# Optimization experiments

Hardware: AMD Instinct MI355X
Metric: run time of the kernel (lower is better)

## Reference

```python
import jax, jax.numpy as jnp
import numpy as np

B = 4096        # graphs
N0 = 32         # nodes per graph
N = B * N0      # 131072 nodes
EP = 128        # edges per graph
E = B * EP      # 524288 edges
H, C = 2, 64    # heads, per-head channels
D = H * C       # 128
K1, K2, K3 = 29, 27, 25  # ceil(0.9*32), ceil(0.9*29), ceil(0.9*27)


def setup_inputs() -> dict:
    key = jax.random.key(0)
    ks = jax.random.split(key, 8)
    x = jax.random.normal(ks[0], (N, 41), jnp.float32)
    g = jnp.repeat(jnp.arange(B, dtype=jnp.int32), EP)
    src = g * N0 + jax.random.randint(ks[1], (E,), 0, N0, jnp.int32)
    dst = g * N0 + jax.random.randint(ks[2], (E,), 0, N0, jnp.int32)
    edge_index = jnp.stack([src, dst])
    edge_attr = jax.random.normal(ks[3], (E, 10), jnp.float32)
    batch = jnp.repeat(jnp.arange(B, dtype=jnp.int32), N0)

    def lin(k, i, o):
        return jax.random.normal(k, (i, o), jnp.float32) / np.float32(np.sqrt(i))

    p = {"x": x, "edge_index": edge_index, "edge_attr": edge_attr, "batch": batch}
    fins = {1: 41, 2: D, 3: D}
    for li in (1, 2, 3):
        sub = jax.random.split(ks[3 + li], 6)
        p[f"W{li}"] = lin(sub[0], fins[li], D)
        p[f"We{li}"] = lin(sub[1], 10, D)
        p[f"as{li}"] = jax.random.normal(sub[2], (H, C), jnp.float32) * 0.1
        p[f"ad{li}"] = jax.random.normal(sub[3], (H, C), jnp.float32) * 0.1
        p[f"ae{li}"] = jax.random.normal(sub[4], (H, C), jnp.float32) * 0.1
        p[f"b{li}"] = jnp.zeros((D,), jnp.float32)
        p[f"g{li}"] = jnp.ones((D,), jnp.float32)
        p[f"be{li}"] = jnp.zeros((D,), jnp.float32)
        p[f"pw{li}"] = jax.random.normal(sub[5], (D,), jnp.float32)
    sub = jax.random.split(ks[7], 2)
    p["fw1"] = lin(sub[0], D, 64)
    p["fb1"] = jnp.zeros((64,), jnp.float32)
    p["fw2"] = lin(sub[1], 64, 1)
    p["fb2"] = jnp.zeros((1,), jnp.float32)
    return p


def gat_conv(x, src, dst, edge_attr, node_mask, edge_mask, W, We, a_s, a_d, a_e, b):
    # PyG GATConv w/ edge_dim, add_self_loops=True, fill_value='mean'
    emf = edge_mask.astype(x.dtype)
    loop_attr = jax.ops.segment_sum(edge_attr * emf[:, None], dst, num_segments=N)
    loop_attr = loop_attr / jnp.maximum(jax.ops.segment_sum(emf, dst, num_segments=N), 1.0)[:, None]
    idx = jnp.arange(N, dtype=src.dtype)
    s = jnp.concatenate([src, idx])
    d = jnp.concatenate([dst, idx])
    ea = jnp.concatenate([edge_attr, loop_attr], axis=0)
    msk = jnp.concatenate([edge_mask, node_mask])
    h = (x @ W).reshape(N, H, C)                       # [N,H,C]
    eh = (ea @ We).reshape(-1, H, C)                   # [E+N,H,C]
    alpha = (h * a_s).sum(-1)[s] + (h * a_d).sum(-1)[d] + (eh * a_e).sum(-1)
    alpha = jax.nn.leaky_relu(alpha, 0.2)              # [E+N,H]
    alpha = jnp.where(msk[:, None], alpha, -1e9)
    mx = jax.ops.segment_max(alpha, d, num_segments=N)  # segment softmax over dst
    p = jnp.where(msk[:, None], jnp.exp(alpha - mx[d]), 0.0)
    den = jax.ops.segment_sum(p, d, num_segments=N)
    w = p / jnp.maximum(den[d], 1e-16)
    out = jax.ops.segment_sum(w[:, :, None] * h[s], d, num_segments=N)
    return out.reshape(N, D) + b


def masked_bn(x, nm, gamma, beta, eps=1e-5):
    m = nm.astype(x.dtype)[:, None]
    n = jnp.maximum(m.sum(), 1.0)
    mu = (x * m).sum(0) / n
    var = (jnp.square(x - mu) * m).sum(0) / n
    return gamma * (x - mu) * jax.lax.rsqrt(var + eps) + beta


def topk_pool(x, w, nm, k):
    sc = (x @ w) / jnp.linalg.norm(w)                  # [N]
    sg = jnp.where(nm, sc, -1e9).reshape(B, N0)
    _, idx = jax.lax.top_k(sg, k)                      # per-graph top-k
    nm2 = jnp.zeros((B, N0), bool).at[jnp.arange(B)[:, None], idx].set(True).reshape(-1)
    xn = jnp.where(nm2[:, None], x * jnp.tanh(sc)[:, None], 0.0)
    return xn, nm2


def graph_mean(x, nm, batch):
    m = nm.astype(x.dtype)
    s = jax.ops.segment_sum(x * m[:, None], batch, num_segments=B)
    c = jax.ops.segment_sum(m, batch, num_segments=B)
    return s / jnp.maximum(c, 1.0)[:, None]


def _forward(x, edge_index, edge_attr, batch,
             W1, We1, as1, ad1, ae1, b1, g1, be1, pw1,
             W2, We2, as2, ad2, ae2, b2, g2, be2, pw2,
             W3, We3, as3, ad3, ae3, b3, g3, be3, pw3,
             fw1, fb1, fw2, fb2):
    src, dst = edge_index[0], edge_index[1]
    nm = jnp.ones((N,), bool)
    em = jnp.ones((E,), bool)
    layers = [(W1, We1, as1, ad1, ae1, b1, g1, be1, pw1, K1),
              (W2, We2, as2, ad2, ae2, b2, g2, be2, pw2, K2),
              (W3, We3, as3, ad3, ae3, b3, g3, be3, pw3, K3)]
    reads = []
    for (W, We, a_s, a_d, a_e, b, g, be, pw, k) in layers:
        x = gat_conv(x, src, dst, edge_attr, nm, em, W, We, a_s, a_d, a_e, b)
        x = jax.nn.relu(masked_bn(x, nm, g, be))
        x, nm = topk_pool(x, pw, nm, k)
        em = em & nm[src] & nm[dst]
        reads.append(graph_mean(x, nm, batch))
    z = reads[0] + reads[1] + reads[2]
    z = jax.nn.relu(z @ fw1 + fb1)
    return z @ fw2 + fb2


def reference(x, edge_index, edge_attr, batch,
              W1, We1, as1, ad1, ae1, b1, g1, be1, pw1,
              W2, We2, as2, ad2, ae2, b2, g2, be2, pw2,
              W3, We3, as3, ad3, ae3, b3, g3, be3, pw3,
              fw1, fb1, fw2, fb2):
    return _forward(x, edge_index, edge_attr, batch,
                    W1, We1, as1, ad1, ae1, b1, g1, be1, pw1,
                    W2, We2, as2, ad2, ae2, b2, g2, be2, pw2,
                    W3, We3, as3, ad3, ae3, b3, g3, be3, pw3,
                    fw1, fb1, fw2, fb2)
```

## Files before the change

### kernel.cpp

```cpp
#include <hip/hip_runtime.h>

#define NN 131072
#define NG 4096
#define NE 524288

__device__ __forceinline__ float lrelu(float a){ return a>=0.f ? a : 0.2f*a; }

template<int K, int PMODE, int KSEL>
__global__ __launch_bounds__(256) void pool_gemm_kernel(
    const float* __restrict__ Xin, float* bufA, unsigned char* nmg,
    const float* __restrict__ stat,
    const float* __restrict__ gamma, const float* __restrict__ beta,
    const float* __restrict__ Wg,
    float* zacc)
{
    constexpr int XP = (K == 41) ? 44 : 132;
    __shared__ float xs[64 * XP];
    __shared__ float scS[64], tsS[64];
    __shared__ int   nmlS[64];

    int tid = threadIdx.x;
    long row0 = (long)blockIdx.x * 64;
    int g0 = blockIdx.x * 2;

    if (PMODE == 0) {
        for (int i = tid; i < 64 * 41; i += 256) {
            int r = i / 41, c = i - r * 41;
            xs[r * 44 + c] = Xin[row0 * 41 + i];
        }
    } else {
        for (int i = tid; i < 2048; i += 256) {
            int r = i >> 5, dc = (i & 31) * 4;
            float4 v = *(const float4*)&bufA[(row0 + r) * 128 + dc];
            v.x = fmaxf(gamma[dc    ] * (v.x - stat[dc    ]) * stat[128 + dc    ] + beta[dc    ], 0.f);
            v.y = fmaxf(gamma[dc + 1] * (v.y - stat[dc + 1]) * stat[128 + dc + 1] + beta[dc + 1], 0.f);
            v.z = fmaxf(gamma[dc + 2] * (v.z - stat[dc + 2]) * stat[128 + dc + 2] + beta[dc + 2], 0.f);
            v.w = fmaxf(gamma[dc + 3] * (v.w - stat[dc + 3]) * stat[128 + dc + 3] + beta[dc + 3], 0.f);
            *(float4*)&xs[r * XP + dc] = v;
        }
        if (tid < 64) nmlS[tid] = (PMODE == 1) ? 1 : (int)nmg[g0 * 32 + tid];
    }
    __syncthreads();

    if (PMODE > 0) {
        {
            int node = tid >> 2, l4 = tid & 3;
            float s = 0.f;
            for (int m = 0; m < 32; m++) { int c = l4 + 4 * m; s += xs[node * XP + c] * stat[256 + c]; }
            s += __shfl_xor(s, 2); s += __shfl_xor(s, 1);
            if (l4 == 0) scS[node] = s;
        }
        __syncthreads();
        if (tid < 64) {
            int gp = tid >> 5, n = tid & 31;
            float sn = nmlS[tid] ? scS[tid] : -1e9f;
            int cnt = 0;
            for (int j = 0; j < 32; j++) {
                float sj = nmlS[gp * 32 + j] ? scS[gp * 32 + j] : -1e9f;
                cnt += (sj > sn || (sj == sn && j < n)) ? 1 : 0;
            }
            int sl = (cnt < KSEL) ? 1 : 0;
            nmg[g0 * 32 + tid] = (unsigned char)sl;
            tsS[tid] = sl ? tanhf(scS[tid]) : 0.f;
        }
        __syncthreads();
        {
            int gp = tid >> 7, d = tid & 127;
            float s = 0.f;
            for (int n = 0; n < 32; n++) s += tsS[gp * 32 + n] * xs[(gp * 32 + n) * XP + d];
            zacc[(long)(g0 + gp) * 128 + d] += s * (1.0f / (float)KSEL);
        }
    }

    int r0 = (tid >> 5) * 8, c4 = (tid & 31) * 4;
    float acc[8][4];
#pragma unroll
    for (int i = 0; i < 8; i++)
#pragma unroll
        for (int j = 0; j < 4; j++) acc[i][j] = 0.f;

    constexpr int KM4 = (K / 4) * 4;
#pragma unroll 4
    for (int k0 = 0; k0 < KM4; k0 += 4) {
        float4 wv0 = *(const float4*)&Wg[(k0 + 0) * 128 + c4];
        float4 wv1 = *(const float4*)&Wg[(k0 + 1) * 128 + c4];
        float4 wv2 = *(const float4*)&Wg[(k0 + 2) * 128 + c4];
        float4 wv3 = *(const float4*)&Wg[(k0 + 3) * 128 + c4];
#pragma unroll
        for (int i = 0; i < 8; i++) {
            float4 xv = *(const float4*)&xs[(r0 + i) * XP + k0];
            acc[i][0] += xv.x * wv0.x + xv.y * wv1.x + xv.z * wv2.x + xv.w * wv3.x;
            acc[i][1] += xv.x * wv0.y + xv.y * wv1.y + xv.z * wv2.y + xv.w * wv3.y;
            acc[i][2] += xv.x * wv0.z + xv.y * wv1.z + xv.z * wv2.z + xv.w * wv3.z;
            acc[i][3] += xv.x * wv0.w + xv.y * wv1.w + xv.z * wv2.w + xv.w * wv3.w;
        }
    }
    for (int k = KM4; k < K; k++) {
        float4 wv = *(const float4*)&Wg[k * 128 + c4];
#pragma unroll
        for (int i = 0; i < 8; i++) {
            float xv = xs[(r0 + i) * XP + k];
            acc[i][0] += xv * wv.x; acc[i][1] += xv * wv.y;
            acc[i][2] += xv * wv.z; acc[i][3] += xv * wv.w;
        }
    }
#pragma unroll
    for (int i = 0; i < 8; i++) {
        float t = 1.f;
        if (PMODE > 0) t = tsS[r0 + i];
        *(float4*)&bufA[(row0 + r0 + i) * 128 + c4] =
            make_float4(acc[i][0] * t, acc[i][1] * t, acc[i][2] * t, acc[i][3] * t);
    }
}

__global__ __launch_bounds__(256) void attn_kernel(
    float* bufA,
    const int* __restrict__ srcp, const int* __restrict__ dstp,
    const float* __restrict__ EA,
    const unsigned char* __restrict__ nmg,
    const float* __restrict__ stat,
    const float* __restrict__ as_, const float* __restrict__ ad_,
    const float* __restrict__ bb,
    float* sums)
{
    __shared__ float hs[32 * 128];
    __shared__ float Wm[2 * 32 * 36];
    __shared__ float scr[320];
    __shared__ unsigned char nmlS[32];

    int g = blockIdx.x, tid = threadIdx.x;
    long gb = (long)g * 4096;

    float ea0 = 0.f, ea1 = 0.f;
    int myls = 0, myld = 0;
    if (tid < 128) {
        myls = srcp[g * 128 + tid] & 31;
        myld = dstp[g * 128 + tid] & 31;
        const float* ep = EA + (long)(g * 128 + tid) * 10;
#pragma unroll
        for (int j = 0; j < 10; j++) { float v = ep[j]; ea0 += v * stat[384 + j]; ea1 += v * stat[394 + j]; }
    }
    for (int i = tid; i < 2304; i += 256) Wm[i] = 0.f;
    if (tid < 96) scr[128 + tid] = 0.f;
    if (tid < 32) nmlS[tid] = nmg[g * 32 + tid];
#pragma unroll
    for (int k = 0; k < 4; k++) {
        int i = tid + 256 * k, r = i >> 5, c4 = i & 31;
        *(float4*)&hs[r * 128 + ((c4 ^ (r & 7)) << 2)] =
            *(const float4*)&bufA[gb + (long)i * 4];
    }
    __syncthreads();

    {
        int node = tid >> 3, l8 = tid & 7, rb = node * 128, k = node & 7;
        float s0 = 0, s1 = 0, d0 = 0, d1 = 0;
#pragma unroll
        for (int m = 0; m < 8; m++) {
            int c = l8 + 8 * m, c4 = c >> 2, j = c & 3;
            int o0 = rb + ((c4 ^ k) << 2) + j;
            float h0 = hs[o0], h1 = hs[o0 + 64];
            s0 += h0 * as_[c];      s1 += h1 * as_[64 + c];
            d0 += h0 * ad_[c];      d1 += h1 * ad_[64 + c];
        }
        s0 += __shfl_xor(s0, 4); s0 += __shfl_xor(s0, 2); s0 += __shfl_xor(s0, 1);
        s1 += __shfl_xor(s1, 4); s1 += __shfl_xor(s1, 2); s1 += __shfl_xor(s1, 1);
        d0 += __shfl_xor(d0, 4); d0 += __shfl_xor(d0, 2); d0 += __shfl_xor(d0, 1);
        d1 += __shfl_xor(d1, 4); d1 += __shfl_xor(d1, 2); d1 += __shfl_xor(d1, 1);
        if (l8 == 0) {
            scr[node * 2] = s0;      scr[node * 2 + 1] = s1;
            scr[64 + node * 2] = d0; scr[64 + node * 2 + 1] = d1;
        }
    }
    int mymk = 0;
    if (tid < 128) {
        mymk = (int)nmlS[myls] & (int)nmlS[myld];
        if (mymk) {
            atomicAdd(&scr[128 + myld * 2], ea0);
            atomicAdd(&scr[128 + myld * 2 + 1], ea1);
            atomicAdd(&scr[192 + myld], 1.f);
        }
    }
    __syncthreads();

    if (tid < 128) {
        if (mymk) {
            float p0 = __expf(lrelu(scr[myls * 2]     + scr[64 + myld * 2]     + ea0));
            float p1 = __expf(lrelu(scr[myls * 2 + 1] + scr[64 + myld * 2 + 1] + ea1));
            atomicAdd(&Wm[myls * 36 + myld], p0);
            atomicAdd(&Wm[1152 + myls * 36 + myld], p1);
        }
    } else if (tid < 192) {
        int t2 = tid - 128, n = t2 >> 1, h = t2 & 1;
        if (nmlS[n]) {
            float c = scr[192 + n]; c = (c > 0.f) ? c : 1.f;
            float ps = __expf(lrelu(scr[n * 2 + h] + scr[64 + n * 2 + h] + scr[128 + n * 2 + h] / c));
            atomicAdd(&Wm[h * 1152 + n * 36 + n], ps);
        }
    }
    __syncthreads();

    if (tid < 64) {
        int n = tid & 31, h = tid >> 5;
        const float* Wh = &Wm[h * 1152 + n];
        float den = 0.f;
#pragma unroll 8
        for (int s = 0; s < 32; s++) den += Wh[s * 36];
        scr[256 + h * 32 + n] = 1.f / fmaxf(den, 1e-16f);
    } else if (tid < 128) {
        *(float4*)&scr[(tid - 64) * 4] = make_float4(0.f, 0.f, 0.f, 0.f);
    }
    __syncthreads();

    {
        int d = tid & 127, h = d >> 6, nb = tid >> 7;
        int c4 = d >> 2, j = d & 3;
        const float* Wh = &Wm[h * 1152 + nb * 16];
        float acc[16];
#pragma unroll
        for (int i = 0; i < 16; i++) acc[i] = 0.f;
        for (int s = 0; s < 32; s++) {
            float hv = hs[s * 128 + ((c4 ^ (s & 7)) << 2) + j];
            float4 w0 = *(const float4*)&Wh[s * 36];
            float4 w1 = *(const float4*)&Wh[s * 36 + 4];
            float4 w2 = *(const float4*)&Wh[s * 36 + 8];
            float4 w3 = *(const float4*)&Wh[s * 36 + 12];
            acc[0]  += w0.x * hv; acc[1]  += w0.y * hv; acc[2]  += w0.z * hv; acc[3]  += w0.w * hv;
            acc[4]  += w1.x * hv; acc[5]  += w1.y * hv; acc[6]  += w1.z * hv; acc[7]  += w1.w * hv;
            acc[8]  += w2.x * hv; acc[9]  += w2.y * hv; acc[10] += w2.z * hv; acc[11] += w2.w * hv;
            acc[12] += w3.x * hv; acc[13] += w3.y * hv; acc[14] += w3.z * hv; acc[15] += w3.w * hv;
        }
        float bv = bb[d];
        float sp = 0.f, sq = 0.f;
#pragma unroll
        for (int i = 0; i < 16; i++) {
            int n = nb * 16 + i;
            float v = acc[i] * scr[256 + h * 32 + n] + bv;
            bufA[gb + n * 128 + d] = v;
            if (nmlS[n]) { sp += v; sq += v * v; }
        }
        atomicAdd(&scr[d], sp);
        atomicAdd(&scr[128 + d], sq);
    }
    __syncthreads();

    if (tid < 128) {
        int rep = (g & 31) * 256;
        atomicAdd(&sums[rep + tid], scr[tid]);
        atomicAdd(&sums[rep + 128 + tid], scr[128 + tid]);
    }
}

__global__ __launch_bounds__(128) void setup_kernel(
    float* sums, float* stat, const float* __restrict__ We, const float* __restrict__ ae)
{
    int t = threadIdx.x;
    for (int i = t; i < 32 * 256; i += 128) sums[i] = 0.f;
    if (t < 20) {
        int h = t / 10, j = t - 10 * h;
        float s = 0.f;
        for (int c = 0; c < 64; c++) s += We[j * 128 + h * 64 + c] * ae[h * 64 + c];
        stat[384 + t] = s;
    }
}

__global__ __launch_bounds__(128) void finalize_kernel(
    float* sums, float n, const float* __restrict__ pw, float* stat,
    const float* __restrict__ Wen, const float* __restrict__ aen)
{
    int d = threadIdx.x;
    float s1 = 0.f, s2 = 0.f;
#pragma unroll
    for (int r = 0; r < 32; r++) { s1 += sums[r * 256 + d]; s2 += sums[r * 256 + 128 + d]; }
    float mean = s1 / n;
    float var = s2 / n - mean * mean;
    if (var < 0.f) var = 0.f;
    float rstd = rsqrtf(var + 1e-5f);
    float p = pw[d];
    float q = p * p;
#pragma unroll
    for (int o = 32; o >= 1; o >>= 1) q += __shfl_xor(q, o);
    __shared__ float w2[2];
    if ((d & 63) == 0) w2[d >> 6] = q;
    __syncthreads();
    float nrm = sqrtf(w2[0] + w2[1]);
    stat[d] = mean; stat[128 + d] = rstd; stat[256 + d] = p / nrm;
    if (d < 20) {
        int h = d / 10, j = d - 10 * h;
        float s = 0.f;
        for (int c = 0; c < 64; c++) s += Wen[j * 128 + h * 64 + c] * aen[h * 64 + c];
        stat[384 + d] = s;
    }
    for (int i = d; i < 32 * 256; i += 128) sums[i] = 0.f;
}

__global__ __launch_bounds__(256) void final_kernel(
    const float* __restrict__ bufA, const unsigned char* __restrict__ nmg,
    const float* __restrict__ stat,
    const float* __restrict__ gamma, const float* __restrict__ beta,
    const float* __restrict__ zacc,
    const float* __restrict__ fw1, const float* __restrict__ fb1,
    const float* __restrict__ fw2, const float* __restrict__ fb2,
    float* __restrict__ out)
{
    __shared__ float xs[32 * 132], zt[128], hred[64], scS[32], tsS[32];
    __shared__ int nmlS[32];
    int g = blockIdx.x, tid = threadIdx.x;
    long gb = (long)g * 4096;

    if (tid < 32) nmlS[tid] = (int)nmg[g * 32 + tid];
    for (int i = tid; i < 1024; i += 256) {
        int r = i >> 5, dc = (i & 31) * 4;
        float4 v = *(const float4*)&bufA[gb + i * 4];
        v.x = fmaxf(gamma[dc    ] * (v.x - stat[dc    ]) * stat[128 + dc    ] + beta[dc    ], 0.f);
        v.y = fmaxf(gamma[dc + 1] * (v.y - stat[dc + 1]) * stat[128 + dc + 1] + beta[dc + 1], 0.f);
        v.z = fmaxf(gamma[dc + 2] * (v.z - stat[dc + 2]) * stat[128 + dc + 2] + beta[dc + 2], 0.f);
        v.w = fmaxf(gamma[dc + 3] * (v.w - stat[dc + 3]) * stat[128 + dc + 3] + beta[dc + 3], 0.f);
        *(float4*)&xs[r * 132 + dc] = v;
    }
    __syncthreads();

    {
        int node = tid >> 3, l8 = tid & 7;
        float s = 0.f;
        for (int m = 0; m < 16; m++) { int c = l8 + 8 * m; s += xs[node * 132 + c] * stat[256 + c]; }
        s += __shfl_xor(s, 4); s += __shfl_xor(s, 2); s += __shfl_xor(s, 1);
        if (l8 == 0) scS[node] = s;
    }
    __syncthreads();

    if (tid < 32) {
        float sn = nmlS[tid] ? scS[tid] : -1e9f;
        int cnt = 0;
        for (int j = 0; j < 32; j++) {
            float sj = nmlS[j] ? scS[j] : -1e9f;
            cnt += (sj > sn || (sj == sn && j < tid)) ? 1 : 0;
        }
        tsS[tid] = (cnt < 25) ? tanhf(scS[tid]) : 0.f;
    }
    __syncthreads();

    if (tid < 128) {
        float s = 0.f;
        for (int n = 0; n < 32; n++) s += xs[n * 132 + tid] * tsS[n];
        zt[tid] = zacc[(long)g * 128 + tid] + s * (1.0f / 25.0f);
    }
    __syncthreads();

    {
        int j = tid >> 2, p = tid & 3;
        float s = 0.f;
        for (int d = p * 32; d < p * 32 + 32; d++) s += zt[d] * fw1[d * 64 + j];
        s += __shfl_xor(s, 1); s += __shfl_xor(s, 2);
        if (p == 0) hred[j] = fmaxf(s + fb1[j], 0.f) * fw2[j];
    }
    __syncthreads();
    if (tid < 64) {
        float v = hred[tid];
#pragma unroll
        for (int o = 32; o >= 1; o >>= 1) v += __shfl_xor(v, o);
        if (tid == 0) out[g] = v + fb2[0];
    }
}

extern "C" void kernel_launch(void* const* d_in, const int* in_sizes, int n_in,
                              void* d_out, int out_size, void* d_ws, size_t ws_size,
                              hipStream_t stream)
{
    const float* X0 = (const float*)d_in[0];
    const int*   EI = (const int*)d_in[1];
    const float* EA = (const float*)d_in[2];
    const int* srcp = EI;
    const int* dstp = EI + NE;

    const float* W1  = (const float*)d_in[4];  const float* We1 = (const float*)d_in[5];
    const float* as1 = (const float*)d_in[6];  const float* ad1 = (const float*)d_in[7];
    const float* ae1 = (const float*)d_in[8];  const float* b1  = (const float*)d_in[9];
    const float* g1  = (const float*)d_in[10]; const float* be1 = (const float*)d_in[11];
    const float* pw1 = (const float*)d_in[12];
    const float* W2  = (const float*)d_in[13]; const float* We2 = (const float*)d_in[14];
    const float* as2 = (const float*)d_in[15]; const float* ad2 = (const float*)d_in[16];
    const float* ae2 = (const float*)d_in[17]; const float* b2  = (const float*)d_in[18];
    const float* g2  = (const float*)d_in[19]; const float* be2 = (const float*)d_in[20];
    const float* pw2 = (const float*)d_in[21];
    const float* W3  = (const float*)d_in[22]; const float* We3 = (const float*)d_in[23];
    const float* as3 = (const float*)d_in[24]; const float* ad3 = (const float*)d_in[25];
    const float* ae3 = (const float*)d_in[26]; const float* b3  = (const float*)d_in[27];
    const float* g3  = (const float*)d_in[28]; const float* be3 = (const float*)d_in[29];
    const float* pw3 = (const float*)d_in[30];
    const float* fw1 = (const float*)d_in[31]; const float* fb1 = (const float*)d_in[32];
    const float* fw2 = (const float*)d_in[33]; const float* fb2 = (const float*)d_in[34];

    float* bufA = (float*)d_ws;
    float* z    = bufA + (size_t)NN * 128;
    float* sums = z + (size_t)NG * 128;
    float* stat = sums + 32 * 256;
    unsigned char* nmg = (unsigned char*)(stat + 512);

    hipMemsetAsync(nmg, 1, NN, stream);
    hipMemsetAsync(z, 0, (size_t)NG * 128 * sizeof(float), stream);
    setup_kernel<<<1, 128, 0, stream>>>(sums, stat, We1, ae1);

    pool_gemm_kernel<41, 0, 1><<<NN / 64, 256, 0, stream>>>(
        X0, bufA, nmg, stat, g1, be1, W1, z);
    attn_kernel<<<NG, 256, 0, stream>>>(bufA, srcp, dstp, EA, nmg, stat, as1, ad1, b1, sums);
    finalize_kernel<<<1, 128, 0, stream>>>(sums, 131072.f, pw1, stat, We2, ae2);

    pool_gemm_kernel<128, 1, 29><<<NN / 64, 256, 0, stream>>>(
        X0, bufA, nmg, stat, g1, be1, W2, z);
    attn_kernel<<<NG, 256, 0, stream>>>(bufA, srcp, dstp, EA, nmg, stat, as2, ad2, b2, sums);
    finalize_kernel<<<1, 128, 0, stream>>>(sums, 4096.f * 29.f, pw2, stat, We3, ae3);

    pool_gemm_kernel<128, 2, 27><<<NN / 64, 256, 0, stream>>>(
        X0, bufA, nmg, stat, g2, be2, W3, z);
    attn_kernel<<<NG, 256, 0, stream>>>(bufA, srcp, dstp, EA, nmg, stat, as3, ad3, b3, sums);
    finalize_kernel<<<1, 128, 0, stream>>>(sums, 4096.f * 27.f, pw3, stat, We3, ae3);

    final_kernel<<<NG, 256, 0, stream>>>(
        bufA, nmg, stat, g3, be3, z, fw1, fb1, fw2, fb2, (float*)d_out);
}
```

Before: 545.1 us.

## Restructure pool GEMM to per-lane rows with wave-uniform scalar weight loads and swizzled LDS

The small GEMM in pool_gemm_kernel now has each lane own one row and each wave own 32 output columns. Because the wave index goes through readfirstlane, the weight reads are wave-uniform and can become scalar loads instead of per-thread float4 global loads. The shared tile drops its padding and uses an XOR swizzle on float4 columns to avoid LDS bank conflicts, and the scoring and readout loops are updated to match. The cost is 32 accumulators per thread, which raises register pressure, and row-per-lane stores of 32 contiguous floats that coalesce less well.

```diff
diff --git a/kernel.cpp b/kernel.cpp
--- a/kernel.cpp
+++ b/kernel.cpp
@@ -14,8 +14,8 @@
     const float* __restrict__ Wg,
     float* zacc)
 {
-    constexpr int XP = (K == 41) ? 44 : 132;
-    __shared__ float xs[64 * XP];
+    constexpr int XSZ = (K == 41) ? 64 * 44 : 64 * 128;
+    __shared__ float xs[XSZ];
     __shared__ float scS[64], tsS[64];
     __shared__ int   nmlS[64];
 
@@ -30,13 +30,13 @@
         }
     } else {
         for (int i = tid; i < 2048; i += 256) {
-            int r = i >> 5, dc = (i & 31) * 4;
+            int r = i >> 5, c4 = i & 31, dc = c4 * 4;
             float4 v = *(const float4*)&bufA[(row0 + r) * 128 + dc];
             v.x = fmaxf(gamma[dc    ] * (v.x - stat[dc    ]) * stat[128 + dc    ] + beta[dc    ], 0.f);
             v.y = fmaxf(gamma[dc + 1] * (v.y - stat[dc + 1]) * stat[128 + dc + 1] + beta[dc + 1], 0.f);
             v.z = fmaxf(gamma[dc + 2] * (v.z - stat[dc + 2]) * stat[128 + dc + 2] + beta[dc + 2], 0.f);
             v.w = fmaxf(gamma[dc + 3] * (v.w - stat[dc + 3]) * stat[128 + dc + 3] + beta[dc + 3], 0.f);
-            *(float4*)&xs[r * XP + dc] = v;
+            *(float4*)&xs[r * 128 + ((c4 ^ (r & 7)) << 2)] = v;
         }
         if (tid < 64) nmlS[tid] = (PMODE == 1) ? 1 : (int)nmg[g0 * 32 + tid];
     }
@@ -44,9 +44,10 @@
 
     if (PMODE > 0) {
         {
-            int node = tid >> 2, l4 = tid & 3;
+            int node = tid >> 2, l4 = tid & 3, kk = node & 7;
             float s = 0.f;
-            for (int m = 0; m < 32; m++) { int c = l4 + 4 * m; s += xs[node * XP + c] * stat[256 + c]; }
+            for (int m = 0; m < 32; m++)
+                s += xs[node * 128 + ((m ^ kk) << 2) + l4] * stat[256 + 4 * m + l4];
             s += __shfl_xor(s, 2); s += __shfl_xor(s, 1);
             if (l4 == 0) scS[node] = s;
         }
@@ -65,51 +66,72 @@
         }
         __syncthreads();
         {
-            int gp = tid >> 7, d = tid & 127;
+            int gp = tid >> 7, d = tid & 127, c4 = d >> 2, j = d & 3;
             float s = 0.f;
-            for (int n = 0; n < 32; n++) s += tsS[gp * 32 + n] * xs[(gp * 32 + n) * XP + d];
+            for (int n = 0; n < 32; n++) {
+                int r = gp * 32 + n;
+                s += tsS[r] * xs[r * 128 + ((c4 ^ (r & 7)) << 2) + j];
+            }
             zacc[(long)(g0 + gp) * 128 + d] += s * (1.0f / (float)KSEL);
         }
     }
 
-    int r0 = (tid >> 5) * 8, c4 = (tid & 31) * 4;
-    float acc[8][4];
-#pragma unroll
-    for (int i = 0; i < 8; i++)
-#pragma unroll
-        for (int j = 0; j < 4; j++) acc[i][j] = 0.f;
+    int lane = tid & 63;
+    int wv = __builtin_amdgcn_readfirstlane(tid >> 6);
+    const float* __restrict__ Wb = Wg + wv * 32;
+
+    float accv[32];
+#pragma unroll
+    for (int c = 0; c < 32; c++) accv[c] = 0.f;
 
     constexpr int KM4 = (K / 4) * 4;
-#pragma unroll 4
+#pragma unroll 2
     for (int k0 = 0; k0 < KM4; k0 += 4) {
-        float4 wv0 = *(const float4*)&Wg[(k0 + 0) * 128 + c4];
-        float4 wv1 = *(const float4*)&Wg[(k0 + 1) * 128 + c4];
-        float4 wv2 = *(const float4*)&Wg[(k0 + 2) * 128 + c4];
-        float4 wv3 = *(const float4*)&Wg[(k0 + 3) * 128 + c4];
-#pragma unroll
-        for (int i = 0; i < 8; i++) {
-            float4 xv = *(const float4*)&xs[(r0 + i) * XP + k0];
-            acc[i][0] += xv.x * wv0.x + xv.y * wv1.x + xv.z * wv2.x + xv.w * wv3.x;
-            acc[i][1] += xv.x * wv0.y + xv.y * wv1.y + xv.z * wv2.y + xv.w * wv3.y;
-            acc[i][2] += xv.x * wv0.z + xv.y * wv1.z + xv.z * wv2.z + xv.w * wv3.z;
-            acc[i][3] += xv.x * wv0.w + xv.y * wv1.w + xv.z * wv2.w + xv.w * wv3.w;
+        float4 xv;
+        if (PMODE == 0) {
+            xv = *(const float4*)&xs[lane * 44 + k0];
+        } else {
+            xv = *(const float4*)&xs[lane * 128 + ((((k0 >> 2) ^ (lane & 7))) << 2)];
+        }
+        {
+            const float* Wr = Wb + (k0 + 0) * 128;
+#pragma unroll
+            for (int c = 0; c < 32; c++) accv[c] += xv.x * Wr[c];
+        }
+        {
+            const float* Wr = Wb + (k0 + 1) * 128;
+#pragma unroll
+            for (int c = 0; c < 32; c++) accv[c] += xv.y * Wr[c];
+        }
+        {
+            const float* Wr = Wb + (k0 + 2) * 128;
+#pragma unroll
+            for (int c = 0; c < 32; c++) accv[c] += xv.z * Wr[c];
+        }
+        {
+            const float* Wr = Wb + (k0 + 3) * 128;
+#pragma unroll
+            for (int c = 0; c < 32; c++) accv[c] += xv.w * Wr[c];
         }
     }
     for (int k = KM4; k < K; k++) {
-        float4 wv = *(const float4*)&Wg[k * 128 + c4];
-#pragma unroll
-        for (int i = 0; i < 8; i++) {
-            float xv = xs[(r0 + i) * XP + k];
-            acc[i][0] += xv * wv.x; acc[i][1] += xv * wv.y;
-            acc[i][2] += xv * wv.z; acc[i][3] += xv * wv.w;
-        }
-    }
-#pragma unroll
-    for (int i = 0; i < 8; i++) {
+        float xk = (PMODE == 0)
+            ? xs[lane * 44 + k]
+            : xs[lane * 128 + (((k >> 2) ^ (lane & 7)) << 2) + (k & 3)];
+        const float* Wr = Wb + k * 128;
+#pragma unroll
+        for (int c = 0; c < 32; c++) accv[c] += xk * Wr[c];
+    }
+
+    {
         float t = 1.f;
-        if (PMODE > 0) t = tsS[r0 + i];
-        *(float4*)&bufA[(row0 + r0 + i) * 128 + c4] =
-            make_float4(acc[i][0] * t, acc[i][1] * t, acc[i][2] * t, acc[i][3] * t);
+        if (PMODE > 0) t = tsS[lane];
+        float* orow = &bufA[(row0 + lane) * 128 + wv * 32];
+#pragma unroll
+        for (int cc = 0; cc < 8; cc++)
+            *(float4*)&orow[cc * 4] = make_float4(
+                accv[cc * 4 + 0] * t, accv[cc * 4 + 1] * t,
+                accv[cc * 4 + 2] * t, accv[cc * 4 + 3] * t);
     }
 }
 
```

Result: slower. 558.2 us (+2.4%).
